# Optimization experiments

Measured on AMD Instinct MI355X. Metric: run time of the kernel, lower is better.

## Reference

```python
import jax, jax.numpy as jnp
import numpy as np

N, DEG, D = 10000, 8, 128      # nodes, fixed out-degree, feature dim
E = N * DEG                    # graph edges = line-graph nodes
L = E * DEG                    # line-graph edges (fixed out-degree => exact)


def setup_inputs() -> dict:
    key = jax.random.key(0)
    kx, k1, k2 = jax.random.split(key, 3)
    rng = np.random.default_rng(0)

    # graph with fixed out-degree, no self-loops
    src = np.repeat(np.arange(N), DEG)                       # sorted by source
    dst = (src + 1 + rng.integers(0, N - 1, size=E)) % N
    edge_index = jnp.asarray(np.stack([src, dst]), dtype=jnp.int32)  # [2, E]

    # line graph: lg edge i -> j iff dst(i) == src(j)  (src(i)!=dst(i) holds for all i)
    # edges with source node v occupy indices v*DEG .. v*DEG+DEG-1
    lg_src = jnp.asarray(np.repeat(np.arange(E), DEG), dtype=jnp.int32)            # [L]
    lg_dst = jnp.asarray((dst[:, None] * DEG + np.arange(DEG)).reshape(-1),
                         dtype=jnp.int32)                                          # [L]

    x = jax.random.normal(kx, (N, D), jnp.float32)
    s = 1.0 / np.sqrt(D)
    ka, kb = jax.random.split(k1)
    W1 = jax.random.uniform(ka, (D, D), jnp.float32, -s, s)
    b1 = jnp.zeros((D,), jnp.float32)
    W2 = jax.random.uniform(kb, (D, D), jnp.float32, -s, s)
    b2 = jnp.zeros((D,), jnp.float32)
    return {"x": x, "edge_index": edge_index, "lg_src": lg_src, "lg_dst": lg_dst,
            "W1": W1, "b1": b1, "W2": W2, "b2": b2}


def reference(x, edge_index, lg_src, lg_dst, W1, b1, W2, b2):
    src, dst = edge_index[0], edge_index[1]
    # line-graph node features: mean of the two endpoint node features  [E, D]
    lgX = 0.5 * (x[src] + x[dst])
    # edge attr of lg edge (i->j) = feature of shared node = dst of source edge i  [L, D]
    edge_attr = x[dst[lg_src]]

    # 3 applications of the same GINEConv (eps=0, add aggregation)
    for _ in range(3):
        msg = jax.nn.relu(lgX[lg_src] + edge_attr)                      # [L, D]
        aggr = jax.ops.segment_sum(msg, lg_dst, num_segments=E)        # [E, D]
        h = lgX + aggr                                                  # (1+eps)*x_i + aggr, eps=0
        lgX = jax.nn.relu(h @ W1 + b1) @ W2 + b2

    # scatter_mean back to graph nodes over dst index, empty nodes -> 0 (matches pad)
    sums = jax.ops.segment_sum(lgX, dst, num_segments=N)               # [N, D]
    cnt = jax.ops.segment_sum(jnp.ones((E,), lgX.dtype), dst, num_segments=N)
    out = jax.nn.relu(sums / jnp.maximum(cnt, 1.0)[:, None])
    # dropout omitted (eval mode)
    return out
```

## Files before the change

kernel.cpp:

```cpp
#include <hip/hip_runtime.h>

#define NN 10000
#define EE 80000
#define DD 128
#define SLOTS 64

typedef short bf16x8 __attribute__((ext_vector_type(8)));
typedef float f32x4 __attribute__((ext_vector_type(4)));

__device__ __forceinline__ float b2f(uint u){ u <<= 16; return __builtin_bit_cast(float, u); }
__device__ __forceinline__ ushort f2b(float f){
  uint u = __builtin_bit_cast(uint, f);
  u += 0x7fffu + ((u >> 16) & 1u);
  return (ushort)(u >> 16);
}
__device__ __forceinline__ uint pack2(float a, float b){
  return (uint)f2b(a) | ((uint)f2b(b) << 16);
}

__global__ __launch_bounds__(256) void k_pre(const float* __restrict__ x, const int* __restrict__ dst,
                                             const float* __restrict__ W1, const float* __restrict__ W2,
                                             ushort* __restrict__ lgX, ushort* __restrict__ Wt,
                                             int* __restrict__ cnt, int* __restrict__ inlist){
  int b = blockIdx.x;
  int tid = threadIdx.x;
  if (b < 5000){
    int i = b * 16 + (tid >> 4);
    int g = tid & 15;
    int s = i >> 3, d = dst[i];
    const float4* xs = (const float4*)(x + s * DD + g * 8);
    const float4* xd = (const float4*)(x + d * DD + g * 8);
    float4 s0 = xs[0], s1 = xs[1], d0 = xd[0], d1 = xd[1];
    uint4 o;
    o.x = pack2(0.5f * (s0.x + d0.x), 0.5f * (s0.y + d0.y));
    o.y = pack2(0.5f * (s0.z + d0.z), 0.5f * (s0.w + d0.w));
    o.z = pack2(0.5f * (s1.x + d1.x), 0.5f * (s1.y + d1.y));
    o.w = pack2(0.5f * (s1.z + d1.z), 0.5f * (s1.w + d1.w));
    *(uint4*)(lgX + i * DD + g * 8) = o;
  } else if (b < 5128){
    int idx = (b - 5000) * 256 + tid;
    int which = idx >> 14;
    int r = idx & 16383;
    int k = r >> 7, n = r & 127;
    const float* W = which ? W2 : W1;
    Wt[which * 16384 + n * DD + k] = f2b(W[r]);
  } else {
    int i = (b - 5128) * 256 + tid;
    if (i < EE){
      int d = dst[i];
      int pos = atomicAdd(&cnt[d], 1);
      if (pos < SLOTS) inlist[d * SLOTS + pos] = i;
    }
  }
}

__global__ __launch_bounds__(256) void k_aggr(const ushort* __restrict__ lgX, const float* __restrict__ x,
                                              const int* __restrict__ cnt, const int* __restrict__ inlist,
                                              float* __restrict__ A){
  int lane = threadIdx.x & 63;
  int v = blockIdx.x * 4 + (threadIdx.x >> 6);
  float2 xv = *(const float2*)(x + v * DD + lane * 2);
  int n = cnt[v]; if (n > SLOTS) n = SLOTS;
  float ax = 0.f, ay = 0.f;
  for (int t = 0; t < n; ++t){
    int e = inlist[v * SLOTS + t];
    uint u = *(const uint*)(lgX + e * DD + lane * 2);
    ax += fmaxf(b2f(u & 0xffffu) + xv.x, 0.f);
    ay += fmaxf(b2f(u >> 16)     + xv.y, 0.f);
  }
  float2 r; r.x = ax; r.y = ay;
  *(float2*)(A + v * DD + lane * 2) = r;
}

__global__ __launch_bounds__(256) void k_final(const ushort* __restrict__ lgX,
                                               const int* __restrict__ cnt, const int* __restrict__ inlist,
                                               float* __restrict__ out){
  int lane = threadIdx.x & 63;
  int v = blockIdx.x * 4 + (threadIdx.x >> 6);
  int n = cnt[v]; if (n > SLOTS) n = SLOTS;
  float ax = 0.f, ay = 0.f;
  for (int t = 0; t < n; ++t){
    int e = inlist[v * SLOTS + t];
    uint u = *(const uint*)(lgX + e * DD + lane * 2);
    ax += b2f(u & 0xffffu);
    ay += b2f(u >> 16);
  }
  float inv = 1.f / (float)(n > 0 ? n : 1);
  float2 r; r.x = fmaxf(ax * inv, 0.f); r.y = fmaxf(ay * inv, 0.f);
  *(float2*)(out + v * DD + lane * 2) = r;
}

__global__ __launch_bounds__(256) void k_gemm(ushort* __restrict__ lgX, const float* __restrict__ A,
                                              const ushort* __restrict__ Wt,
                                              const float* __restrict__ b1, const float* __restrict__ b2){
  __shared__ uint4 smW[2048];
  __shared__ uint4 smT[2048];
  const int tid = threadIdx.x;
  const int lane = tid & 63;
  const int w = tid >> 6;
  const int rlo = lane & 15;
  const int khi = lane >> 4;
  const int row0 = blockIdx.x * 128;
  const bf16x8* smWb = (const bf16x8*)smW;
  const bf16x8* smTb = (const bf16x8*)smT;
  uint* smTu = (uint*)smT;

  #pragma unroll
  for (int it = 0; it < 8; ++it){
    int gi = it * 256 + tid;
    int r = gi >> 4, g = gi & 15;
    smW[r * 16 + (g ^ (r & 7))] = *(const uint4*)(Wt + gi * 8);
  }

  bf16x8 hfrag[2][4];
  #pragma unroll
  for (int mb = 0; mb < 2; ++mb){
    int row = row0 + (2 * w + mb) * 16 + rlo;
    const ushort* lp = lgX + row * DD;
    const float*  ap = A + (row >> 3) * DD;
    #pragma unroll
    for (int s = 0; s < 4; ++s){
      int k0 = s * 32 + khi * 8;
      uint4 lx = *(const uint4*)(lp + k0);
      float4 a0 = *(const float4*)(ap + k0);
      float4 a1 = *(const float4*)(ap + k0 + 4);
      uint uu[4] = {lx.x, lx.y, lx.z, lx.w};
      float av[8] = {a0.x, a0.y, a0.z, a0.w, a1.x, a1.y, a1.z, a1.w};
      uint4 o;
      o.x = pack2(b2f(uu[0] & 0xffffu) + av[0], b2f(uu[0] >> 16) + av[1]);
      o.y = pack2(b2f(uu[1] & 0xffffu) + av[2], b2f(uu[1] >> 16) + av[3]);
      o.z = pack2(b2f(uu[2] & 0xffffu) + av[4], b2f(uu[2] >> 16) + av[5]);
      o.w = pack2(b2f(uu[3] & 0xffffu) + av[6], b2f(uu[3] >> 16) + av[7]);
      hfrag[mb][s] = __builtin_bit_cast(bf16x8, o);
    }
  }
  __syncthreads();

  f32x4 acc1[2][8];
  #pragma unroll
  for (int mb = 0; mb < 2; ++mb)
    #pragma unroll
    for (int nf = 0; nf < 8; ++nf) acc1[mb][nf] = (f32x4){0.f, 0.f, 0.f, 0.f};
  #pragma unroll
  for (int s = 0; s < 4; ++s){
    #pragma unroll
    for (int nf = 0; nf < 8; ++nf){
      int r = nf * 16 + rlo;
      int g = s * 4 + khi;
      bf16x8 wf = smWb[r * 16 + (g ^ (r & 7))];
      acc1[0][nf] = __builtin_amdgcn_mfma_f32_16x16x32_bf16(wf, hfrag[0][s], acc1[0][nf], 0, 0, 0);
      acc1[1][nf] = __builtin_amdgcn_mfma_f32_16x16x32_bf16(wf, hfrag[1][s], acc1[1][nf], 0, 0, 0);
    }
  }

  #pragma unroll
  for (int mb = 0; mb < 2; ++mb){
    int row = (2 * w + mb) * 16 + rlo;
    int rsw = row & 7;
    #pragma unroll
    for (int nf = 0; nf < 8; ++nf){
      float4 bb = *(const float4*)(b1 + nf * 16 + khi * 4);
      float t0 = fmaxf(acc1[mb][nf][0] + bb.x, 0.f);
      float t1 = fmaxf(acc1[mb][nf][1] + bb.y, 0.f);
      float t2 = fmaxf(acc1[mb][nf][2] + bb.z, 0.f);
      float t3 = fmaxf(acc1[mb][nf][3] + bb.w, 0.f);
      int u0 = nf * 8 + khi * 2;
      int g0 = u0 >> 2;
      int base = row * 64 + ((g0 ^ rsw) << 2) + (u0 & 3);
      smTu[base]     = pack2(t0, t1);
      smTu[base + 1] = pack2(t2, t3);
    }
  }

  f32x4 acc2[2][8];
  #pragma unroll
  for (int mb = 0; mb < 2; ++mb)
    #pragma unroll
    for (int nf = 0; nf < 8; ++nf) acc2[mb][nf] = (f32x4){0.f, 0.f, 0.f, 0.f};
  #pragma unroll
  for (int s = 0; s < 4; ++s){
    bf16x8 tf[2];
    #pragma unroll
    for (int mb = 0; mb < 2; ++mb){
      int row = (2 * w + mb) * 16 + rlo;
      int g = s * 4 + khi;
      tf[mb] = smTb[row * 16 + (g ^ (row & 7))];
    }
    #pragma unroll
    for (int nf = 0; nf < 8; ++nf){
      bf16x8 wf = *(const bf16x8*)(Wt + 16384 + (nf * 16 + rlo) * DD + s * 32 + khi * 8);
      acc2[0][nf] = __builtin_amdgcn_mfma_f32_16x16x32_bf16(wf, tf[0], acc2[0][nf], 0, 0, 0);
      acc2[1][nf] = __builtin_amdgcn_mfma_f32_16x16x32_bf16(wf, tf[1], acc2[1][nf], 0, 0, 0);
    }
  }

  #pragma unroll
  for (int mb = 0; mb < 2; ++mb){
    int row = (2 * w + mb) * 16 + rlo;
    int rsw = row & 7;
    #pragma unroll
    for (int nf = 0; nf < 8; ++nf){
      float4 bb = *(const float4*)(b2 + nf * 16 + khi * 4);
      float t0 = acc2[mb][nf][0] + bb.x;
      float t1 = acc2[mb][nf][1] + bb.y;
      float t2 = acc2[mb][nf][2] + bb.z;
      float t3 = acc2[mb][nf][3] + bb.w;
      int u0 = nf * 8 + khi * 2;
      int g0 = u0 >> 2;
      int base = row * 64 + ((g0 ^ rsw) << 2) + (u0 & 3);
      smTu[base]     = pack2(t0, t1);
      smTu[base + 1] = pack2(t2, t3);
    }
  }
  #pragma unroll
  for (int mb = 0; mb < 2; ++mb){
    int row = (2 * w + mb) * 16 + rlo;
    #pragma unroll
    for (int s = 0; s < 4; ++s){
      int g = s * 4 + khi;
      uint4 val = smT[row * 16 + (g ^ (row & 7))];
      *(uint4*)(lgX + (row0 + row) * DD + s * 32 + khi * 8) = val;
    }
  }
}

extern "C" void kernel_launch(void* const* d_in, const int* in_sizes, int n_in,
                              void* d_out, int out_size, void* d_ws, size_t ws_size,
                              hipStream_t stream){
  (void)in_sizes; (void)n_in; (void)out_size; (void)ws_size;
  const float* x  = (const float*)d_in[0];
  const int*   ei = (const int*)d_in[1];
  const int*   dst = ei + EE;
  const float* W1 = (const float*)d_in[4];
  const float* b1 = (const float*)d_in[5];
  const float* W2 = (const float*)d_in[6];
  const float* b2 = (const float*)d_in[7];
  float* out = (float*)d_out;

  char* ws = (char*)d_ws;
  ushort* lgX = (ushort*)ws;
  float*  A   = (float*)(ws + 20480000);
  ushort* Wt  = (ushort*)(ws + 25600000);
  int*    cnt = (int*)(ws + 25665536);
  int*    inl = (int*)(ws + 25705536);

  hipMemsetAsync(cnt, 0, NN * sizeof(int), stream);
  k_pre<<<5441, 256, 0, stream>>>(x, dst, W1, W2, lgX, Wt, cnt, inl);
  for (int it = 0; it < 3; ++it){
    k_aggr<<<NN / 4, 256, 0, stream>>>(lgX, x, cnt, inl, A);
    k_gemm<<<EE / 128, 256, 0, stream>>>(lgX, A, Wt, b1, b2);
  }
  k_final<<<NN / 4, 256, 0, stream>>>(lgX, cnt, inl, out);
}
```

Measured before the change: 229.2 us.

## Fuse all stages into one persistent kernel with software grid barriers

Replaces the eight separate launches (pre, three aggr/gemm pairs, final) with one persistent kernel of 256 blocks. The blocks loop over work units and synchronise between stages through an atomic-counter grid barrier. This removes per-launch overhead and the tail idle time between kernels. The cost is fewer resident blocks (256 on a chip with many CUs) and barrier spin latency, and correctness relies on all 256 blocks being co-resident.

```diff
diff --git a/kernel.cpp b/kernel.cpp
--- a/kernel.cpp
+++ b/kernel.cpp
@@ -4,6 +4,10 @@
 #define EE 80000
 #define DD 128
 #define SLOTS 64
+#define GRID 256
+#define NTILE 625
+#define NVB 2500
+#define NPRE 5441
 
 typedef short bf16x8 __attribute__((ext_vector_type(8)));
 typedef float f32x4 __attribute__((ext_vector_type(4)));
@@ -18,92 +22,68 @@
   return (uint)f2b(a) | ((uint)f2b(b) << 16);
 }
 
-__global__ __launch_bounds__(256) void k_pre(const float* __restrict__ x, const int* __restrict__ dst,
-                                             const float* __restrict__ W1, const float* __restrict__ W2,
-                                             ushort* __restrict__ lgX, ushort* __restrict__ Wt,
-                                             int* __restrict__ cnt, int* __restrict__ inlist){
-  int b = blockIdx.x;
-  int tid = threadIdx.x;
-  if (b < 5000){
-    int i = b * 16 + (tid >> 4);
-    int g = tid & 15;
-    int s = i >> 3, d = dst[i];
-    const float4* xs = (const float4*)(x + s * DD + g * 8);
-    const float4* xd = (const float4*)(x + d * DD + g * 8);
-    float4 s0 = xs[0], s1 = xs[1], d0 = xd[0], d1 = xd[1];
-    uint4 o;
-    o.x = pack2(0.5f * (s0.x + d0.x), 0.5f * (s0.y + d0.y));
-    o.y = pack2(0.5f * (s0.z + d0.z), 0.5f * (s0.w + d0.w));
-    o.z = pack2(0.5f * (s1.x + d1.x), 0.5f * (s1.y + d1.y));
-    o.w = pack2(0.5f * (s1.z + d1.z), 0.5f * (s1.w + d1.w));
-    *(uint4*)(lgX + i * DD + g * 8) = o;
-  } else if (b < 5128){
-    int idx = (b - 5000) * 256 + tid;
-    int which = idx >> 14;
-    int r = idx & 16383;
-    int k = r >> 7, n = r & 127;
-    const float* W = which ? W2 : W1;
-    Wt[which * 16384 + n * DD + k] = f2b(W[r]);
-  } else {
-    int i = (b - 5128) * 256 + tid;
-    if (i < EE){
-      int d = dst[i];
-      int pos = atomicAdd(&cnt[d], 1);
-      if (pos < SLOTS) inlist[d * SLOTS + pos] = i;
-    }
-  }
-}
-
-__global__ __launch_bounds__(256) void k_aggr(const ushort* __restrict__ lgX, const float* __restrict__ x,
-                                              const int* __restrict__ cnt, const int* __restrict__ inlist,
-                                              float* __restrict__ A){
-  int lane = threadIdx.x & 63;
-  int v = blockIdx.x * 4 + (threadIdx.x >> 6);
-  float2 xv = *(const float2*)(x + v * DD + lane * 2);
-  int n = cnt[v]; if (n > SLOTS) n = SLOTS;
-  float ax = 0.f, ay = 0.f;
-  for (int t = 0; t < n; ++t){
-    int e = inlist[v * SLOTS + t];
-    uint u = *(const uint*)(lgX + e * DD + lane * 2);
-    ax += fmaxf(b2f(u & 0xffffu) + xv.x, 0.f);
-    ay += fmaxf(b2f(u >> 16)     + xv.y, 0.f);
-  }
-  float2 r; r.x = ax; r.y = ay;
-  *(float2*)(A + v * DD + lane * 2) = r;
-}
-
-__global__ __launch_bounds__(256) void k_final(const ushort* __restrict__ lgX,
-                                               const int* __restrict__ cnt, const int* __restrict__ inlist,
-                                               float* __restrict__ out){
-  int lane = threadIdx.x & 63;
-  int v = blockIdx.x * 4 + (threadIdx.x >> 6);
-  int n = cnt[v]; if (n > SLOTS) n = SLOTS;
-  float ax = 0.f, ay = 0.f;
-  for (int t = 0; t < n; ++t){
-    int e = inlist[v * SLOTS + t];
-    uint u = *(const uint*)(lgX + e * DD + lane * 2);
-    ax += b2f(u & 0xffffu);
-    ay += b2f(u >> 16);
-  }
-  float inv = 1.f / (float)(n > 0 ? n : 1);
-  float2 r; r.x = fmaxf(ax * inv, 0.f); r.y = fmaxf(ay * inv, 0.f);
-  *(float2*)(out + v * DD + lane * 2) = r;
-}
-
-__global__ __launch_bounds__(256) void k_gemm(ushort* __restrict__ lgX, const float* __restrict__ A,
-                                              const ushort* __restrict__ Wt,
-                                              const float* __restrict__ b1, const float* __restrict__ b2){
+__device__ __forceinline__ void gbar(int* bar, int expect){
+  __syncthreads();
+  __threadfence();
+  if (threadIdx.x == 0){
+    atomicAdd(bar, 1);
+    while (atomicAdd(bar, 0) < expect){ __builtin_amdgcn_s_sleep(8); }
+  }
+  __syncthreads();
+  __threadfence();
+}
+
+__global__ __launch_bounds__(256, 2) void k_all(
+    const float* __restrict__ x, const int* __restrict__ dst,
+    const float* __restrict__ W1, const float* __restrict__ b1,
+    const float* __restrict__ W2, const float* __restrict__ b2,
+    ushort* __restrict__ lgX, float* __restrict__ A, ushort* __restrict__ Wt,
+    int* bar, int* __restrict__ cnt, int* __restrict__ inl, float* __restrict__ out)
+{
   __shared__ uint4 smW[2048];
   __shared__ uint4 smT[2048];
   const int tid = threadIdx.x;
+  const int bid = blockIdx.x;
   const int lane = tid & 63;
   const int w = tid >> 6;
   const int rlo = lane & 15;
   const int khi = lane >> 4;
-  const int row0 = blockIdx.x * 128;
   const bf16x8* smWb = (const bf16x8*)smW;
   const bf16x8* smTb = (const bf16x8*)smT;
   uint* smTu = (uint*)smT;
+  int bexp = 0;
+
+  for (int u = bid; u < NPRE; u += GRID){
+    if (u < 5000){
+      int i = u * 16 + (tid >> 4);
+      int g = tid & 15;
+      int s = i >> 3, d = dst[i];
+      const float4* xs = (const float4*)(x + s * DD + g * 8);
+      const float4* xd = (const float4*)(x + d * DD + g * 8);
+      float4 s0 = xs[0], s1 = xs[1], d0 = xd[0], d1 = xd[1];
+      uint4 o;
+      o.x = pack2(0.5f * (s0.x + d0.x), 0.5f * (s0.y + d0.y));
+      o.y = pack2(0.5f * (s0.z + d0.z), 0.5f * (s0.w + d0.w));
+      o.z = pack2(0.5f * (s1.x + d1.x), 0.5f * (s1.y + d1.y));
+      o.w = pack2(0.5f * (s1.z + d1.z), 0.5f * (s1.w + d1.w));
+      *(uint4*)(lgX + i * DD + g * 8) = o;
+    } else if (u < 5128){
+      int idx = (u - 5000) * 256 + tid;
+      int which = idx >> 14;
+      int r = idx & 16383;
+      int k = r >> 7, n = r & 127;
+      const float* W = which ? W2 : W1;
+      Wt[which * 16384 + n * DD + k] = f2b(W[r]);
+    } else {
+      int i = (u - 5128) * 256 + tid;
+      if (i < EE){
+        int d = dst[i];
+        int pos = atomicAdd(&cnt[d], 1);
+        if (pos < SLOTS) inl[d * SLOTS + pos] = i;
+      }
+    }
+  }
+  bexp += GRID; gbar(bar, bexp);
 
   #pragma unroll
   for (int it = 0; it < 8; ++it){
@@ -112,115 +92,154 @@
     smW[r * 16 + (g ^ (r & 7))] = *(const uint4*)(Wt + gi * 8);
   }
 
-  bf16x8 hfrag[2][4];
-  #pragma unroll
-  for (int mb = 0; mb < 2; ++mb){
-    int row = row0 + (2 * w + mb) * 16 + rlo;
-    const ushort* lp = lgX + row * DD;
-    const float*  ap = A + (row >> 3) * DD;
-    #pragma unroll
-    for (int s = 0; s < 4; ++s){
-      int k0 = s * 32 + khi * 8;
-      uint4 lx = *(const uint4*)(lp + k0);
-      float4 a0 = *(const float4*)(ap + k0);
-      float4 a1 = *(const float4*)(ap + k0 + 4);
-      uint uu[4] = {lx.x, lx.y, lx.z, lx.w};
-      float av[8] = {a0.x, a0.y, a0.z, a0.w, a1.x, a1.y, a1.z, a1.w};
-      uint4 o;
-      o.x = pack2(b2f(uu[0] & 0xffffu) + av[0], b2f(uu[0] >> 16) + av[1]);
-      o.y = pack2(b2f(uu[1] & 0xffffu) + av[2], b2f(uu[1] >> 16) + av[3]);
-      o.z = pack2(b2f(uu[2] & 0xffffu) + av[4], b2f(uu[2] >> 16) + av[5]);
-      o.w = pack2(b2f(uu[3] & 0xffffu) + av[6], b2f(uu[3] >> 16) + av[7]);
-      hfrag[mb][s] = __builtin_bit_cast(bf16x8, o);
-    }
-  }
-  __syncthreads();
-
-  f32x4 acc1[2][8];
-  #pragma unroll
-  for (int mb = 0; mb < 2; ++mb)
-    #pragma unroll
-    for (int nf = 0; nf < 8; ++nf) acc1[mb][nf] = (f32x4){0.f, 0.f, 0.f, 0.f};
-  #pragma unroll
-  for (int s = 0; s < 4; ++s){
-    #pragma unroll
-    for (int nf = 0; nf < 8; ++nf){
-      int r = nf * 16 + rlo;
-      int g = s * 4 + khi;
-      bf16x8 wf = smWb[r * 16 + (g ^ (r & 7))];
-      acc1[0][nf] = __builtin_amdgcn_mfma_f32_16x16x32_bf16(wf, hfrag[0][s], acc1[0][nf], 0, 0, 0);
-      acc1[1][nf] = __builtin_amdgcn_mfma_f32_16x16x32_bf16(wf, hfrag[1][s], acc1[1][nf], 0, 0, 0);
-    }
-  }
-
-  #pragma unroll
-  for (int mb = 0; mb < 2; ++mb){
-    int row = (2 * w + mb) * 16 + rlo;
-    int rsw = row & 7;
-    #pragma unroll
-    for (int nf = 0; nf < 8; ++nf){
-      float4 bb = *(const float4*)(b1 + nf * 16 + khi * 4);
-      float t0 = fmaxf(acc1[mb][nf][0] + bb.x, 0.f);
-      float t1 = fmaxf(acc1[mb][nf][1] + bb.y, 0.f);
-      float t2 = fmaxf(acc1[mb][nf][2] + bb.z, 0.f);
-      float t3 = fmaxf(acc1[mb][nf][3] + bb.w, 0.f);
-      int u0 = nf * 8 + khi * 2;
-      int g0 = u0 >> 2;
-      int base = row * 64 + ((g0 ^ rsw) << 2) + (u0 & 3);
-      smTu[base]     = pack2(t0, t1);
-      smTu[base + 1] = pack2(t2, t3);
-    }
-  }
-
-  f32x4 acc2[2][8];
-  #pragma unroll
-  for (int mb = 0; mb < 2; ++mb)
-    #pragma unroll
-    for (int nf = 0; nf < 8; ++nf) acc2[mb][nf] = (f32x4){0.f, 0.f, 0.f, 0.f};
-  #pragma unroll
-  for (int s = 0; s < 4; ++s){
-    bf16x8 tf[2];
-    #pragma unroll
-    for (int mb = 0; mb < 2; ++mb){
-      int row = (2 * w + mb) * 16 + rlo;
-      int g = s * 4 + khi;
-      tf[mb] = smTb[row * 16 + (g ^ (row & 7))];
-    }
-    #pragma unroll
-    for (int nf = 0; nf < 8; ++nf){
-      bf16x8 wf = *(const bf16x8*)(Wt + 16384 + (nf * 16 + rlo) * DD + s * 32 + khi * 8);
-      acc2[0][nf] = __builtin_amdgcn_mfma_f32_16x16x32_bf16(wf, tf[0], acc2[0][nf], 0, 0, 0);
-      acc2[1][nf] = __builtin_amdgcn_mfma_f32_16x16x32_bf16(wf, tf[1], acc2[1][nf], 0, 0, 0);
-    }
-  }
-
-  #pragma unroll
-  for (int mb = 0; mb < 2; ++mb){
-    int row = (2 * w + mb) * 16 + rlo;
-    int rsw = row & 7;
-    #pragma unroll
-    for (int nf = 0; nf < 8; ++nf){
-      float4 bb = *(const float4*)(b2 + nf * 16 + khi * 4);
-      float t0 = acc2[mb][nf][0] + bb.x;
-      float t1 = acc2[mb][nf][1] + bb.y;
-      float t2 = acc2[mb][nf][2] + bb.z;
-      float t3 = acc2[mb][nf][3] + bb.w;
-      int u0 = nf * 8 + khi * 2;
-      int g0 = u0 >> 2;
-      int base = row * 64 + ((g0 ^ rsw) << 2) + (u0 & 3);
-      smTu[base]     = pack2(t0, t1);
-      smTu[base + 1] = pack2(t2, t3);
-    }
-  }
-  #pragma unroll
-  for (int mb = 0; mb < 2; ++mb){
-    int row = (2 * w + mb) * 16 + rlo;
-    #pragma unroll
-    for (int s = 0; s < 4; ++s){
-      int g = s * 4 + khi;
-      uint4 val = smT[row * 16 + (g ^ (row & 7))];
-      *(uint4*)(lgX + (row0 + row) * DD + s * 32 + khi * 8) = val;
-    }
+  for (int iter = 0; iter < 3; ++iter){
+    for (int vb = bid; vb < NVB; vb += GRID){
+      int v = vb * 4 + (tid >> 6);
+      float2 xv = *(const float2*)(x + v * DD + lane * 2);
+      int n = cnt[v]; if (n > SLOTS) n = SLOTS;
+      float ax = 0.f, ay = 0.f;
+      const int* ip = inl + v * SLOTS;
+      for (int t = 0; t < n; ++t){
+        int e = ip[t];
+        uint u = *(const uint*)(lgX + e * DD + lane * 2);
+        ax += fmaxf(b2f(u & 0xffffu) + xv.x, 0.f);
+        ay += fmaxf(b2f(u >> 16)     + xv.y, 0.f);
+      }
+      float2 r; r.x = ax; r.y = ay;
+      *(float2*)(A + v * DD + lane * 2) = r;
+    }
+    bexp += GRID; gbar(bar, bexp);
+
+    for (int tb = bid; tb < NTILE; tb += GRID){
+      const int row0 = tb * 128;
+
+      bf16x8 hfrag[2][4];
+      #pragma unroll
+      for (int mb = 0; mb < 2; ++mb){
+        int row = row0 + (2 * w + mb) * 16 + rlo;
+        const ushort* lp = lgX + row * DD;
+        const float*  ap = A + (row >> 3) * DD;
+        #pragma unroll
+        for (int s = 0; s < 4; ++s){
+          int k0 = s * 32 + khi * 8;
+          uint4 lx = *(const uint4*)(lp + k0);
+          float4 a0 = *(const float4*)(ap + k0);
+          float4 a1 = *(const float4*)(ap + k0 + 4);
+          uint uu[4] = {lx.x, lx.y, lx.z, lx.w};
+          float av[8] = {a0.x, a0.y, a0.z, a0.w, a1.x, a1.y, a1.z, a1.w};
+          uint4 o;
+          o.x = pack2(b2f(uu[0] & 0xffffu) + av[0], b2f(uu[0] >> 16) + av[1]);
+          o.y = pack2(b2f(uu[1] & 0xffffu) + av[2], b2f(uu[1] >> 16) + av[3]);
+          o.z = pack2(b2f(uu[2] & 0xffffu) + av[4], b2f(uu[2] >> 16) + av[5]);
+          o.w = pack2(b2f(uu[3] & 0xffffu) + av[6], b2f(uu[3] >> 16) + av[7]);
+          hfrag[mb][s] = __builtin_bit_cast(bf16x8, o);
+        }
+      }
+
+      f32x4 acc1[2][8];
+      #pragma unroll
+      for (int mb = 0; mb < 2; ++mb)
+        #pragma unroll
+        for (int nf = 0; nf < 8; ++nf) acc1[mb][nf] = (f32x4){0.f, 0.f, 0.f, 0.f};
+      #pragma unroll
+      for (int s = 0; s < 4; ++s){
+        #pragma unroll
+        for (int nf = 0; nf < 8; ++nf){
+          int r = nf * 16 + rlo;
+          int g = s * 4 + khi;
+          bf16x8 wf = smWb[r * 16 + (g ^ (r & 7))];
+          acc1[0][nf] = __builtin_amdgcn_mfma_f32_16x16x32_bf16(wf, hfrag[0][s], acc1[0][nf], 0, 0, 0);
+          acc1[1][nf] = __builtin_amdgcn_mfma_f32_16x16x32_bf16(wf, hfrag[1][s], acc1[1][nf], 0, 0, 0);
+        }
+      }
+
+      #pragma unroll
+      for (int mb = 0; mb < 2; ++mb){
+        int row = (2 * w + mb) * 16 + rlo;
+        int rsw = row & 7;
+        #pragma unroll
+        for (int nf = 0; nf < 8; ++nf){
+          float4 bb = *(const float4*)(b1 + nf * 16 + khi * 4);
+          float t0 = fmaxf(acc1[mb][nf][0] + bb.x, 0.f);
+          float t1 = fmaxf(acc1[mb][nf][1] + bb.y, 0.f);
+          float t2 = fmaxf(acc1[mb][nf][2] + bb.z, 0.f);
+          float t3 = fmaxf(acc1[mb][nf][3] + bb.w, 0.f);
+          int u0 = nf * 8 + khi * 2;
+          int g0 = u0 >> 2;
+          int base = row * 64 + ((g0 ^ rsw) << 2) + (u0 & 3);
+          smTu[base]     = pack2(t0, t1);
+          smTu[base + 1] = pack2(t2, t3);
+        }
+      }
+
+      f32x4 acc2[2][8];
+      #pragma unroll
+      for (int mb = 0; mb < 2; ++mb)
+        #pragma unroll
+        for (int nf = 0; nf < 8; ++nf) acc2[mb][nf] = (f32x4){0.f, 0.f, 0.f, 0.f};
+      #pragma unroll
+      for (int s = 0; s < 4; ++s){
+        bf16x8 tf[2];
+        #pragma unroll
+        for (int mb = 0; mb < 2; ++mb){
+          int row = (2 * w + mb) * 16 + rlo;
+          int g = s * 4 + khi;
+          tf[mb] = smTb[row * 16 + (g ^ (row & 7))];
+        }
+        #pragma unroll
+        for (int nf = 0; nf < 8; ++nf){
+          bf16x8 wf = *(const bf16x8*)(Wt + 16384 + (nf * 16 + rlo) * DD + s * 32 + khi * 8);
+          acc2[0][nf] = __builtin_amdgcn_mfma_f32_16x16x32_bf16(wf, tf[0], acc2[0][nf], 0, 0, 0);
+          acc2[1][nf] = __builtin_amdgcn_mfma_f32_16x16x32_bf16(wf, tf[1], acc2[1][nf], 0, 0, 0);
+        }
+      }
+
+      #pragma unroll
+      for (int mb = 0; mb < 2; ++mb){
+        int row = (2 * w + mb) * 16 + rlo;
+        int rsw = row & 7;
+        #pragma unroll
+        for (int nf = 0; nf < 8; ++nf){
+          float4 bb = *(const float4*)(b2 + nf * 16 + khi * 4);
+          float t0 = acc2[mb][nf][0] + bb.x;
+          float t1 = acc2[mb][nf][1] + bb.y;
+          float t2 = acc2[mb][nf][2] + bb.z;
+          float t3 = acc2[mb][nf][3] + bb.w;
+          int u0 = nf * 8 + khi * 2;
+          int g0 = u0 >> 2;
+          int base = row * 64 + ((g0 ^ rsw) << 2) + (u0 & 3);
+          smTu[base]     = pack2(t0, t1);
+          smTu[base + 1] = pack2(t2, t3);
+        }
+      }
+      #pragma unroll
+      for (int mb = 0; mb < 2; ++mb){
+        int row = (2 * w + mb) * 16 + rlo;
+        #pragma unroll
+        for (int s = 0; s < 4; ++s){
+          int g = s * 4 + khi;
+          uint4 val = smT[row * 16 + (g ^ (row & 7))];
+          *(uint4*)(lgX + (row0 + row) * DD + s * 32 + khi * 8) = val;
+        }
+      }
+    }
+    bexp += GRID; gbar(bar, bexp);
+  }
+
+  for (int vb = bid; vb < NVB; vb += GRID){
+    int v = vb * 4 + (tid >> 6);
+    int n = cnt[v]; if (n > SLOTS) n = SLOTS;
+    float ax = 0.f, ay = 0.f;
+    const int* ip = inl + v * SLOTS;
+    for (int t = 0; t < n; ++t){
+      int e = ip[t];
+      uint u = *(const uint*)(lgX + e * DD + lane * 2);
+      ax += b2f(u & 0xffffu);
+      ay += b2f(u >> 16);
+    }
+    float inv = 1.f / (float)(n > 0 ? n : 1);
+    float2 r; r.x = fmaxf(ax * inv, 0.f); r.y = fmaxf(ay * inv, 0.f);
+    *(float2*)(out + v * DD + lane * 2) = r;
   }
 }
 
@@ -241,14 +260,10 @@
   ushort* lgX = (ushort*)ws;
   float*  A   = (float*)(ws + 20480000);
   ushort* Wt  = (ushort*)(ws + 25600000);
-  int*    cnt = (int*)(ws + 25665536);
-  int*    inl = (int*)(ws + 25705536);
-
-  hipMemsetAsync(cnt, 0, NN * sizeof(int), stream);
-  k_pre<<<5441, 256, 0, stream>>>(x, dst, W1, W2, lgX, Wt, cnt, inl);
-  for (int it = 0; it < 3; ++it){
-    k_aggr<<<NN / 4, 256, 0, stream>>>(lgX, x, cnt, inl, A);
-    k_gemm<<<EE / 128, 256, 0, stream>>>(lgX, A, Wt, b1, b2);
-  }
-  k_final<<<NN / 4, 256, 0, stream>>>(lgX, cnt, inl, out);
-}
+  int*    bar = (int*)(ws + 25665536);
+  int*    cnt = (int*)(ws + 25665568);
+  int*    inl = (int*)(ws + 25705568);
+
+  hipMemsetAsync(bar, 0, 32 + NN * sizeof(int), stream);
+  k_all<<<GRID, 256, 0, stream>>>(x, dst, W1, b1, W2, b2, lgX, A, Wt, bar, cnt, inl, out);
+}
```

Result: slower. 860.0 us (+275.2%).

## Reorder line-graph rows by destination node into CSR for contiguous aggregation

Applied to the files above, without the earlier changes.

Builds a CSR ordering of edges by destination node (count, scan, scatter) and stores lgX rows in that permuted order. Aggregation and final mean then read contiguous rows instead of gathering through an index list, and the GEMM looks up each row's source node through srcOf. It adds three small setup kernels, including a single-block serial scan, plus an indirect index load in the GEMM. It also removes the 64-slot cap on in-degree.

```diff
diff --git a/kernel.cpp b/kernel.cpp
--- a/kernel.cpp
+++ b/kernel.cpp
@@ -3,7 +3,6 @@
 #define NN 10000
 #define EE 80000
 #define DD 128
-#define SLOTS 64
 
 typedef short bf16x8 __attribute__((ext_vector_type(8)));
 typedef float f32x4 __attribute__((ext_vector_type(4)));
@@ -18,79 +17,106 @@
   return (uint)f2b(a) | ((uint)f2b(b) << 16);
 }
 
-__global__ __launch_bounds__(256) void k_pre(const float* __restrict__ x, const int* __restrict__ dst,
-                                             const float* __restrict__ W1, const float* __restrict__ W2,
-                                             ushort* __restrict__ lgX, ushort* __restrict__ Wt,
-                                             int* __restrict__ cnt, int* __restrict__ inlist){
-  int b = blockIdx.x;
-  int tid = threadIdx.x;
-  if (b < 5000){
-    int i = b * 16 + (tid >> 4);
-    int g = tid & 15;
-    int s = i >> 3, d = dst[i];
-    const float4* xs = (const float4*)(x + s * DD + g * 8);
-    const float4* xd = (const float4*)(x + d * DD + g * 8);
-    float4 s0 = xs[0], s1 = xs[1], d0 = xd[0], d1 = xd[1];
-    uint4 o;
-    o.x = pack2(0.5f * (s0.x + d0.x), 0.5f * (s0.y + d0.y));
-    o.y = pack2(0.5f * (s0.z + d0.z), 0.5f * (s0.w + d0.w));
-    o.z = pack2(0.5f * (s1.x + d1.x), 0.5f * (s1.y + d1.y));
-    o.w = pack2(0.5f * (s1.z + d1.z), 0.5f * (s1.w + d1.w));
-    *(uint4*)(lgX + i * DD + g * 8) = o;
-  } else if (b < 5128){
-    int idx = (b - 5000) * 256 + tid;
+__global__ __launch_bounds__(256) void k_prep(const float* __restrict__ W1, const float* __restrict__ W2,
+                                              const int* __restrict__ dst,
+                                              ushort* __restrict__ Wt, int* __restrict__ cnt){
+  int b = blockIdx.x, tid = threadIdx.x;
+  if (b < 128){
+    int idx = b * 256 + tid;
     int which = idx >> 14;
     int r = idx & 16383;
     int k = r >> 7, n = r & 127;
     const float* W = which ? W2 : W1;
     Wt[which * 16384 + n * DD + k] = f2b(W[r]);
   } else {
-    int i = (b - 5128) * 256 + tid;
-    if (i < EE){
-      int d = dst[i];
-      int pos = atomicAdd(&cnt[d], 1);
-      if (pos < SLOTS) inlist[d * SLOTS + pos] = i;
-    }
-  }
+    int i = (b - 128) * 256 + tid;
+    if (i < EE) atomicAdd(&cnt[dst[i]], 1);
+  }
+}
+
+__global__ __launch_bounds__(256) void k_scan(const int* __restrict__ cnt,
+                                              int* __restrict__ start, int* __restrict__ pos){
+  __shared__ int part[256];
+  int t = threadIdx.x;
+  int c0 = t * 40, c1 = c0 + 40; if (c1 > NN) c1 = NN; if (c0 > NN) c0 = NN;
+  int s = 0;
+  for (int i = c0; i < c1; ++i) s += cnt[i];
+  part[t] = s;
+  __syncthreads();
+  if (t == 0){
+    int acc = 0;
+    for (int i = 0; i < 256; ++i){ int v = part[i]; part[i] = acc; acc += v; }
+  }
+  __syncthreads();
+  int acc = part[t];
+  for (int i = c0; i < c1; ++i){ start[i] = acc; pos[i] = acc; acc += cnt[i]; }
+  if (t == 255) start[NN] = EE;
+}
+
+__global__ __launch_bounds__(256) void k_build(const int* __restrict__ dst, int* __restrict__ pos,
+                                               int* __restrict__ srcOf, int* __restrict__ dstOf){
+  int i = blockIdx.x * 256 + threadIdx.x;
+  if (i < EE){
+    int d = dst[i];
+    int slot = atomicAdd(&pos[d], 1);
+    srcOf[slot] = i >> 3;
+    dstOf[slot] = d;
+  }
+}
+
+__global__ __launch_bounds__(256) void k_init(const float* __restrict__ x,
+                                              const int* __restrict__ srcOf, const int* __restrict__ dstOf,
+                                              ushort* __restrict__ lgX){
+  int tid = threadIdx.x;
+  int r = blockIdx.x * 16 + (tid >> 4);
+  int g = tid & 15;
+  int s = srcOf[r], d = dstOf[r];
+  const float4* xs = (const float4*)(x + s * DD + g * 8);
+  const float4* xd = (const float4*)(x + d * DD + g * 8);
+  float4 s0 = xs[0], s1 = xs[1], d0 = xd[0], d1 = xd[1];
+  uint4 o;
+  o.x = pack2(0.5f * (s0.x + d0.x), 0.5f * (s0.y + d0.y));
+  o.y = pack2(0.5f * (s0.z + d0.z), 0.5f * (s0.w + d0.w));
+  o.z = pack2(0.5f * (s1.x + d1.x), 0.5f * (s1.y + d1.y));
+  o.w = pack2(0.5f * (s1.z + d1.z), 0.5f * (s1.w + d1.w));
+  *(uint4*)(lgX + r * DD + g * 8) = o;
 }
 
 __global__ __launch_bounds__(256) void k_aggr(const ushort* __restrict__ lgX, const float* __restrict__ x,
-                                              const int* __restrict__ cnt, const int* __restrict__ inlist,
-                                              float* __restrict__ A){
+                                              const int* __restrict__ start, float* __restrict__ A){
   int lane = threadIdx.x & 63;
   int v = blockIdx.x * 4 + (threadIdx.x >> 6);
   float2 xv = *(const float2*)(x + v * DD + lane * 2);
-  int n = cnt[v]; if (n > SLOTS) n = SLOTS;
+  int r0 = start[v], r1 = start[v + 1];
   float ax = 0.f, ay = 0.f;
-  for (int t = 0; t < n; ++t){
-    int e = inlist[v * SLOTS + t];
-    uint u = *(const uint*)(lgX + e * DD + lane * 2);
+  for (int r = r0; r < r1; ++r){
+    uint u = *(const uint*)(lgX + r * DD + lane * 2);
     ax += fmaxf(b2f(u & 0xffffu) + xv.x, 0.f);
     ay += fmaxf(b2f(u >> 16)     + xv.y, 0.f);
   }
-  float2 r; r.x = ax; r.y = ay;
-  *(float2*)(A + v * DD + lane * 2) = r;
+  float2 rr; rr.x = ax; rr.y = ay;
+  *(float2*)(A + v * DD + lane * 2) = rr;
 }
 
 __global__ __launch_bounds__(256) void k_final(const ushort* __restrict__ lgX,
-                                               const int* __restrict__ cnt, const int* __restrict__ inlist,
-                                               float* __restrict__ out){
+                                               const int* __restrict__ start, float* __restrict__ out){
   int lane = threadIdx.x & 63;
   int v = blockIdx.x * 4 + (threadIdx.x >> 6);
-  int n = cnt[v]; if (n > SLOTS) n = SLOTS;
+  int r0 = start[v], r1 = start[v + 1];
+  int n = r1 - r0;
   float ax = 0.f, ay = 0.f;
-  for (int t = 0; t < n; ++t){
-    int e = inlist[v * SLOTS + t];
-    uint u = *(const uint*)(lgX + e * DD + lane * 2);
+  for (int r = r0; r < r1; ++r){
+    uint u = *(const uint*)(lgX + r * DD + lane * 2);
     ax += b2f(u & 0xffffu);
     ay += b2f(u >> 16);
   }
   float inv = 1.f / (float)(n > 0 ? n : 1);
-  float2 r; r.x = fmaxf(ax * inv, 0.f); r.y = fmaxf(ay * inv, 0.f);
-  *(float2*)(out + v * DD + lane * 2) = r;
+  float2 rr; rr.x = fmaxf(ax * inv, 0.f); rr.y = fmaxf(ay * inv, 0.f);
+  *(float2*)(out + v * DD + lane * 2) = rr;
 }
 
 __global__ __launch_bounds__(256) void k_gemm(ushort* __restrict__ lgX, const float* __restrict__ A,
+                                              const int* __restrict__ srcOf,
                                               const ushort* __restrict__ Wt,
                                               const float* __restrict__ b1, const float* __restrict__ b2){
   __shared__ uint4 smW[2048];
@@ -117,7 +143,7 @@
   for (int mb = 0; mb < 2; ++mb){
     int row = row0 + (2 * w + mb) * 16 + rlo;
     const ushort* lp = lgX + row * DD;
-    const float*  ap = A + (row >> 3) * DD;
+    const float*  ap = A + srcOf[row] * DD;
     #pragma unroll
     for (int s = 0; s < 4; ++s){
       int k0 = s * 32 + khi * 8;
@@ -238,17 +264,23 @@
   float* out = (float*)d_out;
 
   char* ws = (char*)d_ws;
-  ushort* lgX = (ushort*)ws;
-  float*  A   = (float*)(ws + 20480000);
-  ushort* Wt  = (ushort*)(ws + 25600000);
-  int*    cnt = (int*)(ws + 25665536);
-  int*    inl = (int*)(ws + 25705536);
+  ushort* lgX   = (ushort*)ws;
+  float*  A     = (float*)(ws + 20480000);
+  ushort* Wt    = (ushort*)(ws + 25600000);
+  int*    start = (int*)(ws + 25665536);
+  int*    pos   = (int*)(ws + 25706496);
+  int*    cnt   = (int*)(ws + 25746496);
+  int*    srcOf = (int*)(ws + 25786496);
+  int*    dstOf = (int*)(ws + 26106496);
 
   hipMemsetAsync(cnt, 0, NN * sizeof(int), stream);
-  k_pre<<<5441, 256, 0, stream>>>(x, dst, W1, W2, lgX, Wt, cnt, inl);
+  k_prep<<<441, 256, 0, stream>>>(W1, W2, dst, Wt, cnt);
+  k_scan<<<1, 256, 0, stream>>>(cnt, start, pos);
+  k_build<<<313, 256, 0, stream>>>(dst, pos, srcOf, dstOf);
+  k_init<<<EE / 16, 256, 0, stream>>>(x, srcOf, dstOf, lgX);
   for (int it = 0; it < 3; ++it){
-    k_aggr<<<NN / 4, 256, 0, stream>>>(lgX, x, cnt, inl, A);
-    k_gemm<<<EE / 128, 256, 0, stream>>>(lgX, A, Wt, b1, b2);
-  }
-  k_final<<<NN / 4, 256, 0, stream>>>(lgX, cnt, inl, out);
-}
+    k_aggr<<<NN / 4, 256, 0, stream>>>(lgX, x, start, A);
+    k_gemm<<<EE / 128, 256, 0, stream>>>(lgX, A, srcOf, Wt, b1, b2);
+  }
+  k_final<<<NN / 4, 256, 0, stream>>>(lgX, start, out);
+}
```

New measurement: 255.9 us. 11.6% more time.
